# Kernel tuning notes

Hardware: AMD Instinct MI355X
Metric: run time of the kernel (lower is better)

The kernel has to match this reference:

```python
import jax, jax.numpy as jnp
import numpy as np

INPUT_CHANNELS = 64
OUT_CHANNELS = 64
OUT_DIM = 4
IN_FEAT = INPUT_CHANNELS * OUT_DIM * 2   # 512
OUT_FEAT = OUT_CHANNELS * OUT_DIM        # 256
BATCH = 65536


def setup_inputs() -> dict:
    key = jax.random.key(0)
    k_x, k_w, k_b = jax.random.split(key, 3)
    x = jax.random.normal(k_x, (BATCH, IN_FEAT), dtype=jnp.float32)
    weight = jax.random.normal(k_w, (OUT_FEAT, IN_FEAT), dtype=jnp.float32)
    bias = jax.random.normal(k_b, (1, OUT_FEAT), dtype=jnp.float32)
    return {"x": x, "weight": weight, "bias": bias}


def reference(x, weight, bias) -> jnp.ndarray:
    # Original: (x[:, None] * weight).sum(-1) / sqrt(input_channels) + 0.1*bias
    # Mathematically identical to a GEMM: x @ weight.T
    scale = 1.0 / jnp.sqrt(jnp.asarray(INPUT_CHANNELS, dtype=x.dtype))
    out = jnp.einsum('bi,oi->bo', x, weight) * scale  # [B, out_feat]
    out = out + bias * 0.1
    return out
```

## Files before the change

kernel.cpp:

```cpp
#include <hip/hip_runtime.h>
#include <hip/hip_bf16.h>


typedef __bf16 bf16;
typedef __attribute__((ext_vector_type(8))) __bf16 bf16x8;
typedef __attribute__((ext_vector_type(4))) __bf16 bf16x4;
typedef __attribute__((ext_vector_type(4))) float f32x4;

#define BATCH_ 65536
#define KDIM   512
#define NDIM   256
#define NHALF  128
#define CHUNK_ROWS 16
#define CHUNKS 8
#define ROWS_PER_BLOCK (CHUNK_ROWS * CHUNKS)

__global__ __launch_bounds__(256) void wcvt_kernel(const float* __restrict__ w,
                                                   bf16* __restrict__ wb) {
    int i = (blockIdx.x * 256 + threadIdx.x) * 4;
    f32x4 v = *(const f32x4*)(w + i);
    bf16x4 o;
    o[0] = (bf16)(v.x * 0.125f);
    o[1] = (bf16)(v.y * 0.125f);
    o[2] = (bf16)(v.z * 0.125f);
    o[3] = (bf16)(v.w * 0.125f);
    *(bf16x4*)(wb + i) = o;
}

__device__ __forceinline__ void stage_issue(const float* xc, int tid, f32x4 (&r)[4]) {
#pragma unroll
    for (int i = 0; i < 4; ++i)
        r[i] = *(const f32x4*)((const char*)xc + i * 8192 + tid * 16);
}

__device__ __forceinline__ void stage_write(bf16* buf, int tid, const f32x4 (&r)[4]) {
#pragma unroll
    for (int i = 0; i < 4; ++i) {
        const int row = i * 4 + (tid >> 7);
        const int off = (tid & 127) * 8;
        const int phys = row * 1024 + (off ^ ((row & 7) << 4));
        bf16x4 o;
        o[0] = (bf16)r[i].x;
        o[1] = (bf16)r[i].y;
        o[2] = (bf16)r[i].z;
        o[3] = (bf16)r[i].w;
        *(bf16x4*)((char*)buf + phys) = o;
    }
}

__device__ __forceinline__ void compute_chunk(const bf16* buf, const bf16x8 (&wf)[16],
                                              int l16, int q, f32x4& acc) {
    acc = (f32x4)0.0f;
    const char* base = (const char*)buf + l16 * 1024;
    const int xo = (l16 & 7) << 4;
#pragma unroll
    for (int kc = 0; kc < 16; ++kc) {
        bf16x8 a = *(const bf16x8*)(base + ((kc * 64 + q * 16) ^ xo));
        acc = __builtin_amdgcn_mfma_f32_16x16x32_bf16(a, wf[kc], acc, 0, 0, 0);
    }
}

__global__ __launch_bounds__(512, 4) void gemm_kernel(const float* __restrict__ x,
                                                      const bf16* __restrict__ wb,
                                                      const float* __restrict__ bias,
                                                      float* __restrict__ out) {
    __shared__ __align__(16) bf16 bufA[CHUNK_ROWS * KDIM];
    __shared__ __align__(16) bf16 bufB[CHUNK_ROWS * KDIM];

    const int tid  = threadIdx.x;
    const int lane = tid & 63;
    const int w    = tid >> 6;
    const int q    = lane >> 4;
    const int l16  = lane & 15;
    const int half = blockIdx.x & 1;
    const long rb  = blockIdx.x >> 1;
    const int n0   = half * NHALF + w * 16;
    const long row_base = rb * ROWS_PER_BLOCK;

    bf16x8 wf[16];
#pragma unroll
    for (int kc = 0; kc < 16; ++kc)
        wf[kc] = *(const bf16x8*)(wb + (long)(n0 + l16) * KDIM + kc * 32 + q * 8);
    const float bv = 0.1f * bias[n0 + l16];

    const float* xblk = x + row_base * KDIM;

    {
        f32x4 r0[4];
        stage_issue(xblk, tid, r0);
        stage_write(bufA, tid, r0);
    }
    __syncthreads();

    f32x4 acc;
    f32x4 r[4];
#pragma unroll 1
    for (int t = 0; t < CHUNKS; t += 2) {
        if (t + 1 < CHUNKS)
            stage_issue(xblk + (long)(t + 1) * CHUNK_ROWS * KDIM, tid, r);
        compute_chunk(bufA, wf, l16, q, acc);
        if (t + 1 < CHUNKS)
            stage_write(bufB, tid, r);
        __syncthreads();
        {
            const long row0 = row_base + (long)t * CHUNK_ROWS;
#pragma unroll
            for (int rr = 0; rr < 4; ++rr)
                out[(row0 + q * 4 + rr) * NDIM + n0 + l16] = acc[rr] + bv;
        }

        if (t + 2 < CHUNKS)
            stage_issue(xblk + (long)(t + 2) * CHUNK_ROWS * KDIM, tid, r);
        compute_chunk(bufB, wf, l16, q, acc);
        if (t + 2 < CHUNKS)
            stage_write(bufA, tid, r);
        __syncthreads();
        {
            const long row0 = row_base + (long)(t + 1) * CHUNK_ROWS;
#pragma unroll
            for (int rr = 0; rr < 4; ++rr)
                out[(row0 + q * 4 + rr) * NDIM + n0 + l16] = acc[rr] + bv;
        }
    }
}

extern "C" void kernel_launch(void* const* d_in, const int* in_sizes, int n_in,
                              void* d_out, int out_size, void* d_ws, size_t ws_size,
                              hipStream_t stream) {
    const float* x    = (const float*)d_in[0];
    const float* w    = (const float*)d_in[1];
    const float* bias = (const float*)d_in[2];
    float* out = (float*)d_out;
    bf16* wb   = (bf16*)d_ws;

    wcvt_kernel<<<(NDIM * KDIM) / (256 * 4), 256, 0, stream>>>(w, wb);
    gemm_kernel<<<(BATCH_ / ROWS_PER_BLOCK) * 2, 512, 0, stream>>>(x, wb, bias, out);
}
```

Before: 230.2 us.

## Deepen global prefetch to two chunks, remap blocks, and use lighter LDS barriers

Result: no change. 234.2 us (+1.8%).

```diff
diff --git a/kernel.cpp b/kernel.cpp
--- a/kernel.cpp
+++ b/kernel.cpp
@@ -60,6 +60,12 @@
     }
 }
 
+__device__ __forceinline__ void lds_barrier() {
+    asm volatile("s_waitcnt lgkmcnt(0)" ::: "memory");
+    __builtin_amdgcn_s_barrier();
+    __builtin_amdgcn_sched_barrier(0);
+}
+
 __global__ __launch_bounds__(512, 4) void gemm_kernel(const float* __restrict__ x,
                                                       const bf16* __restrict__ wb,
                                                       const float* __restrict__ bias,
@@ -72,8 +78,10 @@
     const int w    = tid >> 6;
     const int q    = lane >> 4;
     const int l16  = lane & 15;
-    const int half = blockIdx.x & 1;
-    const long rb  = blockIdx.x >> 1;
+
+    const int g    = blockIdx.x;
+    const int half = (g >> 3) & 1;
+    const long rb  = (long)((g & 7) | ((g >> 4) << 3));
     const int n0   = half * NHALF + w * 16;
     const long row_base = rb * ROWS_PER_BLOCK;
 
@@ -85,23 +93,20 @@
 
     const float* xblk = x + row_base * KDIM;
 
-    {
-        f32x4 r0[4];
-        stage_issue(xblk, tid, r0);
-        stage_write(bufA, tid, r0);
-    }
-    __syncthreads();
+    f32x4 rA[4], rB[4];
+    stage_issue(xblk, tid, rA);
+    stage_issue(xblk + 1 * CHUNK_ROWS * KDIM, tid, rB);
+    stage_write(bufA, tid, rA);
+    lds_barrier();
 
     f32x4 acc;
-    f32x4 r[4];
 #pragma unroll 1
     for (int t = 0; t < CHUNKS; t += 2) {
-        if (t + 1 < CHUNKS)
-            stage_issue(xblk + (long)(t + 1) * CHUNK_ROWS * KDIM, tid, r);
+        if (t + 2 < CHUNKS)
+            stage_issue(xblk + (long)(t + 2) * CHUNK_ROWS * KDIM, tid, rA);
         compute_chunk(bufA, wf, l16, q, acc);
-        if (t + 1 < CHUNKS)
-            stage_write(bufB, tid, r);
-        __syncthreads();
+        stage_write(bufB, tid, rB);
+        lds_barrier();
         {
             const long row0 = row_base + (long)t * CHUNK_ROWS;
 #pragma unroll
@@ -109,12 +114,12 @@
                 out[(row0 + q * 4 + rr) * NDIM + n0 + l16] = acc[rr] + bv;
         }
 
-        if (t + 2 < CHUNKS)
-            stage_issue(xblk + (long)(t + 2) * CHUNK_ROWS * KDIM, tid, r);
+        if (t + 3 < CHUNKS)
+            stage_issue(xblk + (long)(t + 3) * CHUNK_ROWS * KDIM, tid, rB);
         compute_chunk(bufB, wf, l16, q, acc);
         if (t + 2 < CHUNKS)
-            stage_write(bufA, tid, r);
-        __syncthreads();
+            stage_write(bufA, tid, rA);
+        lds_barrier();
         {
             const long row0 = row_base + (long)(t + 1) * CHUNK_ROWS;
 #pragma unroll
```
